# Kernel tuning notes

Measured on AMD Instinct MI355X. Metric: run time of the kernel, lower is better.

The kernel has to match this reference:

```python
import jax, jax.numpy as jnp
import numpy as np

N, E, IN, ED, HID, B, K = 50000, 800000, 128, 64, 256, 128, 1000


def setup_inputs() -> dict:
    key = jax.random.key(0)
    ks = jax.random.split(key, 16)

    def lin(k, fi, fo):
        k1, k2 = jax.random.split(k)
        s = 1.0 / np.sqrt(fi)
        return (jax.random.uniform(k1, (fi, fo), jnp.float32, -s, s),
                jax.random.uniform(k2, (fo,), jnp.float32, -s, s))

    We, be = lin(ks[0], ED, IN)        # GINEConv edge projection edge_dim -> in_channels
    W1, b1 = lin(ks[1], IN, HID)       # GINE nn layer 1
    W2, b2 = lin(ks[2], HID, HID)      # GINE nn layer 2
    Wg1, bg1 = lin(ks[3], HID, 128)    # gate_nn layer 1
    Wg2, bg2 = lin(ks[4], 128, 1)      # gate_nn layer 2
    Wh, bh = lin(ks[5], HID, K)        # head

    x = jax.random.normal(ks[6], (N, IN), jnp.float32)
    edge_index = jax.random.randint(ks[7], (2, E), 0, N, jnp.int64)
    edge_attr = jax.random.normal(ks[8], (E, ED), jnp.float32)
    batch = jnp.sort(jax.random.randint(ks[9], (N,), 0, B, jnp.int64))

    return {"x": x, "edge_index": edge_index, "edge_attr": edge_attr, "batch": batch,
            "We": We, "be": be, "W1": W1, "b1": b1, "W2": W2, "b2": b2,
            "Wg1": Wg1, "bg1": bg1, "Wg2": Wg2, "bg2": bg2, "Wh": Wh, "bh": bh}


def reference(x, edge_index, edge_attr, batch, We, be, W1, b1, W2, b2,
              Wg1, bg1, Wg2, bg2, Wh, bh):
    src, dst = edge_index[0], edge_index[1]
    # GINEConv message: ReLU(x_j + Lin(edge_attr)), scatter-add to dst (eps=0)
    e = edge_attr @ We + be                      # [E, IN]
    m = jax.nn.relu(x[src] + e)                  # [E, IN]
    agg = jax.ops.segment_sum(m, dst, num_segments=N)  # [N, IN]
    h = x + agg                                  # (1+eps)*x + agg, eps=0
    h = jax.nn.relu(h @ W1 + b1) @ W2 + b2       # [N, HID]
    # GlobalAttention: segment softmax of gate over graphs, weighted sum
    gate = jax.nn.relu(h @ Wg1 + bg1) @ Wg2 + bg2            # [N, 1]
    gmax = jax.ops.segment_max(gate, batch, num_segments=B)  # [B, 1]
    a = jnp.exp(gate - gmax[batch])
    denom = jax.ops.segment_sum(a, batch, num_segments=B)    # [B, 1]
    attn = a / denom[batch]
    pooled = jax.ops.segment_sum(attn * h, batch, num_segments=B)  # [B, HID]
    logits = pooled @ Wh + bh                    # [B, K]
    return (logits, pooled)
```

## Files before the change

### kernel.cpp

```cpp
#include <hip/hip_runtime.h>
#include <stdint.h>

#define NN    50000
#define EE    800000
#define IN_C  128
#define ED_C  64
#define HID_C 256
#define BB    128
#define KK    1000
#define G1_C  128
#define NV    50176


typedef __attribute__((ext_vector_type(8))) short bfrag;
typedef __attribute__((ext_vector_type(4))) float f4acc;

__device__ __forceinline__ unsigned short f2bs(float f){
  unsigned u = __float_as_uint(f);
  return (unsigned short)((u + 0x7fffu + ((u >> 16) & 1u)) >> 16);
}
__device__ __forceinline__ float bs2f(unsigned short s){
  return __uint_as_float(((unsigned)s) << 16);
}

__device__ __forceinline__ void atomicMaxFloat(float* addr, float val){
  int old = __float_as_int(*addr);
  while (__int_as_float(old) < val){
    int assumed = old;
    old = atomicCAS((int*)addr, assumed, __float_as_int(val));
    if (old == assumed) break;
  }
}

__global__ __launch_bounds__(256) void k_prep(
    const float* __restrict__ We, const float* __restrict__ W1,
    const float* __restrict__ W2, const float* __restrict__ Wg1,
    unsigned short* __restrict__ Wet, unsigned short* __restrict__ W1t,
    unsigned short* __restrict__ W2t, unsigned short* __restrict__ Wg1t)
{
  int i = blockIdx.x * 256 + threadIdx.x;
  if (i < 128 * 64){ int c = i >> 6, k = i & 63;  Wet[i]  = f2bs(We[k * 128 + c]); }
  if (i < 256 * 128){ int n = i >> 7, k = i & 127; W1t[i]  = f2bs(W1[k * 256 + n]); }
  if (i < 256 * 256){ int n = i >> 8, k = i & 255; W2t[i]  = f2bs(W2[k * 256 + n]); }
  if (i < 128 * 256){ int n = i >> 8, k = i & 255; Wg1t[i] = f2bs(Wg1[k * 128 + n]); }
}

__global__ __launch_bounds__(256) void k_init(float* __restrict__ agg,
                                              int* __restrict__ cnt,
                                              int* __restrict__ fill,
                                              int* __restrict__ aux,
                                              float* __restrict__ gmax,
                                              float* __restrict__ denom,
                                              float* __restrict__ pooled){
  size_t i = (size_t)blockIdx.x * 256 + threadIdx.x;
  if (i < (size_t)NN * IN_C) agg[i] = 0.f;
  if (i < NV){ cnt[i] = 0; fill[i] = 0; }
  if (i < 256) aux[i] = 0;
  if (i < BB){ gmax[i] = -1e30f; denom[i] = 0.f; }
  if (i < BB * HID_C) pooled[i] = 0.f;
}

__global__ __launch_bounds__(256) void k_hist(const int* __restrict__ ei,
                                              int* __restrict__ cnt){
  int e = blockIdx.x * 256 + threadIdx.x;
  if (e < EE) atomicAdd(&cnt[ei[EE + e]], 1);
}

__global__ __launch_bounds__(256) void k_scan1(const int* __restrict__ cnt,
                                               int* __restrict__ off,
                                               int* __restrict__ aux){
  __shared__ int s[256];
  int t = threadIdx.x, i = blockIdx.x * 256 + t;
  int val = cnt[i];
  s[t] = val; __syncthreads();
#pragma unroll
  for (int o = 1; o < 256; o <<= 1){
    int v = (t >= o) ? s[t - o] : 0;
    __syncthreads();
    s[t] += v;
    __syncthreads();
  }
  off[i] = s[t] - val;
  if (t == 255) aux[blockIdx.x] = s[255];
}

__global__ __launch_bounds__(256) void k_scan2(int* __restrict__ aux){
  __shared__ int s[256];
  int t = threadIdx.x;
  int val = aux[t];
  s[t] = val; __syncthreads();
#pragma unroll
  for (int o = 1; o < 256; o <<= 1){
    int v = (t >= o) ? s[t - o] : 0;
    __syncthreads();
    s[t] += v;
    __syncthreads();
  }
  aux[t] = s[t] - val;
}

__global__ __launch_bounds__(256) void k_scan3(int* __restrict__ off,
                                               const int* __restrict__ aux){
  int i = blockIdx.x * 256 + threadIdx.x;
  off[i] += aux[blockIdx.x];
}

__global__ __launch_bounds__(256) void k_scatter(const int* __restrict__ ei,
                                                 const int* __restrict__ off,
                                                 int* __restrict__ fill,
                                                 uint4* __restrict__ sorted){
  int e = blockIdx.x * 256 + threadIdx.x;
  if (e < EE){
    int s = ei[e], d = ei[EE + e];
    int pos = off[d] + atomicAdd(&fill[d], 1);
    sorted[pos] = make_uint4((unsigned)e, (unsigned)s, (unsigned)d, 0u);
  }
}

__global__ __launch_bounds__(256, 2) void k_edge2(
    const float* __restrict__ x, const uint4* __restrict__ sorted,
    const float* __restrict__ edge_attr,
    const unsigned short* __restrict__ Wet, const float* __restrict__ be,
    float* __restrict__ agg)
{
  __shared__ float msgS[128 * 132];
  __shared__ uint4 sE[128];
  __shared__ unsigned long long maskS[2];
  __shared__ int runStart[132];
  __shared__ int nRunsS;
  unsigned short* eaS = (unsigned short*)msgS;

  const int tid = threadIdx.x;
  const int e0 = blockIdx.x * 128;
  if (tid < 128) sE[tid] = sorted[e0 + tid];
  __syncthreads();

  const int xrow = tid >> 1;
  const int xc0 = (tid & 1) * 64;
  const float* xptr = x + (size_t)((int)sE[xrow].y) * IN_C + xc0;
  float4 xr[16];
#pragma unroll
  for (int j = 0; j < 16; ++j) xr[j] = *(const float4*)(xptr + j * 4);

  if (tid < 128){
    bool flag = (tid == 0) || ((int)sE[tid].z != (int)sE[tid - 1].z);
    unsigned long long m = __ballot(flag);
    if ((tid & 63) == 0) maskS[tid >> 6] = m;
  }

#pragma unroll
  for (int t = 0; t < 8; ++t){
    int f4 = t * 256 + tid;
    int er = f4 >> 4;
    int kk = (f4 & 15) * 4;
    int eid = (int)sE[er].x;
    const float4 v = *(const float4*)(edge_attr + (size_t)eid * ED_C + kk);
    unsigned p0 = (unsigned)f2bs(v.x) | ((unsigned)f2bs(v.y) << 16);
    unsigned p1 = (unsigned)f2bs(v.z) | ((unsigned)f2bs(v.w) << 16);
    *(uint2*)&eaS[er * 72 + kk] = make_uint2(p0, p1);
  }
  __syncthreads();

  if (tid < 128){
    int lane = tid & 63, wvi = tid >> 6;
    unsigned long long mw = maskS[wvi];
    int pre = __popcll(mw & ((1ull << lane) - 1ull)) + (wvi ? __popcll(maskS[0]) : 0);
    if ((mw >> lane) & 1ull) runStart[pre] = tid;
    if (tid == 0){
      int nr = __popcll(maskS[0]) + __popcll(maskS[1]);
      nRunsS = nr;
      runStart[nr] = 128;
    }
  }

  const int lane = tid & 63, wv = tid >> 6;
  const int q = lane >> 4, l15 = lane & 15;

  f4acc acc[2][8];
  const f4acc zz = {0.f, 0.f, 0.f, 0.f};
#pragma unroll
  for (int mt = 0; mt < 2; ++mt)
#pragma unroll
    for (int nt = 0; nt < 8; ++nt) acc[mt][nt] = zz;

#pragma unroll
  for (int ks = 0; ks < 2; ++ks){
    bfrag a[2], b[8];
#pragma unroll
    for (int mt = 0; mt < 2; ++mt){
      int m = wv * 32 + mt * 16 + l15;
      a[mt] = *(const bfrag*)&eaS[m * 72 + ks * 32 + q * 8];
    }
#pragma unroll
    for (int nt = 0; nt < 8; ++nt){
      int c = nt * 16 + l15;
      b[nt] = *(const bfrag*)(Wet + c * ED_C + ks * 32 + q * 8);
    }
#pragma unroll
    for (int mt = 0; mt < 2; ++mt)
#pragma unroll
      for (int nt = 0; nt < 8; ++nt)
        acc[mt][nt] = __builtin_amdgcn_mfma_f32_16x16x32_bf16(a[mt], b[nt], acc[mt][nt], 0, 0, 0);
  }

  float bev[8];
#pragma unroll
  for (int nt = 0; nt < 8; ++nt) bev[nt] = be[nt * 16 + l15];

  __syncthreads();

#pragma unroll
  for (int mt = 0; mt < 2; ++mt){
    const int g = wv * 32 + mt * 16 + q * 4;
#pragma unroll
    for (int nt = 0; nt < 8; ++nt){
      int c = nt * 16 + l15;
#pragma unroll
      for (int r = 0; r < 4; ++r)
        msgS[(g + r) * 132 + c] = acc[mt][nt][r] + bev[nt];
    }
  }
  __syncthreads();

  {
    float* mr = &msgS[xrow * 132 + xc0];
#pragma unroll
    for (int j = 0; j < 16; ++j){
      float4 w = *(float4*)(mr + j * 4);
      const float4 v = xr[j];
      w.x = fmaxf(w.x + v.x, 0.f);
      w.y = fmaxf(w.y + v.y, 0.f);
      w.z = fmaxf(w.z + v.z, 0.f);
      w.w = fmaxf(w.w + v.w, 0.f);
      *(float4*)(mr + j * 4) = w;
    }
  }
  __syncthreads();

  {
    const int col = tid & 127;
    const int h = tid >> 7;
    const int nR = nRunsS;
    for (int i = h; i < nR; i += 2){
      int s = runStart[i], e = runStart[i + 1];
      int dst = (int)sE[s].z;
      float run = 0.f;
      for (int r = s; r < e; ++r) run += msgS[r * 132 + col];
      size_t a = (size_t)dst * IN_C + col;
      if (s == 0 || e == 128) atomicAdd(&agg[a], run);
      else                    agg[a] = run;
    }
  }
}

__global__ __launch_bounds__(256) void k_h0(const float* __restrict__ agg,
                                            const float* __restrict__ x,
                                            unsigned short* __restrict__ h0b){
  int i = blockIdx.x * 256 + threadIdx.x;
  if (i < NN * IN_C) h0b[i] = f2bs(agg[i] + x[i]);
}

template<int K, bool RELU, bool OF32, bool OB16>
__global__ __launch_bounds__(256) void k_gemm(
    const unsigned short* __restrict__ A, const unsigned short* __restrict__ Wt,
    const float* __restrict__ bias, float* __restrict__ outf,
    unsigned short* __restrict__ outb, int M, int Ntot)
{
  __shared__ unsigned short aS[64 * 40];
  __shared__ unsigned short bS[128 * 40];
  const int tid = threadIdx.x;
  const int lane = tid & 63, wv = tid >> 6;
  const int wi = wv >> 1, wj = wv & 1;
  const int q = lane >> 4, l15 = lane & 15;
  const int mb0 = blockIdx.x * 64;
  const int nb0 = blockIdx.y * 128;
  const int arow = tid >> 2, achk = tid & 3;

  f4acc acc[2][4];
  const f4acc zz = {0.f, 0.f, 0.f, 0.f};
#pragma unroll
  for (int mt = 0; mt < 2; ++mt)
#pragma unroll
    for (int nt = 0; nt < 4; ++nt) acc[mt][nt] = zz;

  for (int ks = 0; ks < K / 32; ++ks){
    {
      int m = mb0 + arow; if (m >= M) m = M - 1;
      const uint4 v = *(const uint4*)(A + (size_t)m * K + ks * 32 + achk * 8);
      *(uint4*)&aS[arow * 40 + achk * 8] = v;
    }
#pragma unroll
    for (int i = 0; i < 2; ++i){
      int idx = i * 256 + tid;
      int row = idx >> 2, chk = idx & 3;
      const uint4 v = *(const uint4*)(Wt + (size_t)(nb0 + row) * K + ks * 32 + chk * 8);
      *(uint4*)&bS[row * 40 + chk * 8] = v;
    }
    __syncthreads();
    bfrag a[2], b[4];
#pragma unroll
    for (int mt = 0; mt < 2; ++mt)
      a[mt] = *(const bfrag*)&aS[(wi * 32 + mt * 16 + l15) * 40 + q * 8];
#pragma unroll
    for (int nt = 0; nt < 4; ++nt)
      b[nt] = *(const bfrag*)&bS[(wj * 64 + nt * 16 + l15) * 40 + q * 8];
#pragma unroll
    for (int mt = 0; mt < 2; ++mt)
#pragma unroll
      for (int nt = 0; nt < 4; ++nt)
        acc[mt][nt] = __builtin_amdgcn_mfma_f32_16x16x32_bf16(a[mt], b[nt], acc[mt][nt], 0, 0, 0);
    __syncthreads();
  }

  const int mb = mb0 + wi * 32;
  const int nb = nb0 + wj * 64;
#pragma unroll
  for (int nt = 0; nt < 4; ++nt){
    int c = nb + nt * 16 + l15;
    float bv = bias[c];
#pragma unroll
    for (int mt = 0; mt < 2; ++mt){
#pragma unroll
      for (int r = 0; r < 4; ++r){
        int m = mb + mt * 16 + q * 4 + r;
        if (m < M){
          float v = acc[mt][nt][r] + bv;
          if (RELU) v = v > 0.f ? v : 0.f;
          if (OF32) outf[(size_t)m * Ntot + c] = v;
          if (OB16) outb[(size_t)m * Ntot + c] = f2bs(v);
        }
      }
    }
  }
}

__global__ __launch_bounds__(256) void k_gate2(const float* __restrict__ g1,
                                               const float* __restrict__ Wg2,
                                               const float* __restrict__ bg2,
                                               float* __restrict__ gate, int nrows){
  const int lane = threadIdx.x & 63, wv = threadIdx.x >> 6;
  const float2 w2 = *(const float2*)(Wg2 + lane * 2);
  const float bg = bg2[0];
  for (int r = blockIdx.x * 4 + wv; r < nrows; r += gridDim.x * 4){
    const float2 a2 = *(const float2*)(g1 + (size_t)r * G1_C + lane * 2);
    float p = a2.x * w2.x + a2.y * w2.y;
#pragma unroll
    for (int off = 32; off > 0; off >>= 1) p += __shfl_down(p, off);
    if (lane == 0) gate[r] = p + bg;
  }
}

__global__ __launch_bounds__(256) void k_gmax(const float* __restrict__ gate,
                                              const int* __restrict__ batch,
                                              float* __restrict__ gmax, int nrows){
  __shared__ float red[256];
  const int tid = threadIdx.x;
  const int n0 = blockIdx.x * 256;
  const int n = n0 + tid;
  const int nlast = (n0 + 255 < nrows) ? n0 + 255 : nrows - 1;
  const int bmin = batch[n0], bmax = batch[nlast];
  float val = -3e38f; int b = bmax;
  if (n < nrows){ b = batch[n]; val = gate[n]; }
  for (int bb = bmin; bb <= bmax; ++bb){
    red[tid] = (b == bb) ? val : -3e38f;
    __syncthreads();
    for (int s = 128; s > 0; s >>= 1){
      if (tid < s) red[tid] = fmaxf(red[tid], red[tid + s]);
      __syncthreads();
    }
    if (tid == 0 && red[0] > -1e37f) atomicMaxFloat(&gmax[bb], red[0]);
    __syncthreads();
  }
}

__global__ __launch_bounds__(256) void k_expsum(const float* __restrict__ gate,
                                                const int* __restrict__ batch,
                                                const float* __restrict__ gmax,
                                                float* __restrict__ aexp,
                                                float* __restrict__ denom, int nrows){
  __shared__ float red[256];
  const int tid = threadIdx.x;
  const int n0 = blockIdx.x * 256;
  const int n = n0 + tid;
  const int nlast = (n0 + 255 < nrows) ? n0 + 255 : nrows - 1;
  const int bmin = batch[n0], bmax = batch[nlast];
  float val = 0.f; int b = bmax;
  if (n < nrows){
    b = batch[n];
    val = expf(gate[n] - gmax[b]);
    aexp[n] = val;
  }
  for (int bb = bmin; bb <= bmax; ++bb){
    red[tid] = (b == bb) ? val : 0.f;
    __syncthreads();
    for (int s = 128; s > 0; s >>= 1){
      if (tid < s) red[tid] += red[tid + s];
      __syncthreads();
    }
    if (tid == 0 && red[0] != 0.f) atomicAdd(&denom[bb], red[0]);
    __syncthreads();
  }
}

__global__ __launch_bounds__(256) void k_pool(const unsigned short* __restrict__ h2b,
                                              const float* __restrict__ aexp,
                                              const float* __restrict__ denom,
                                              const int* __restrict__ batch,
                                              float* __restrict__ pooled, int nrows){
  const int c = threadIdx.x;
  const int n0 = blockIdx.x * 256;
  int n1 = n0 + 256; if (n1 > nrows) n1 = nrows;
  float acc = 0.f;
  int curb = batch[n0];
  for (int n = n0; n < n1; ++n){
    int b = batch[n];
    if (b != curb){
      atomicAdd(&pooled[(size_t)curb * HID_C + c], acc);
      acc = 0.f; curb = b;
    }
    float wgt = aexp[n] / denom[b];
    acc = fmaf(wgt, bs2f(h2b[(size_t)n * HID_C + c]), acc);
  }
  atomicAdd(&pooled[(size_t)curb * HID_C + c], acc);
}

__global__ __launch_bounds__(256) void k_head(const float* __restrict__ pooled,
                                              const float* __restrict__ Wh,
                                              const float* __restrict__ bh,
                                              float* __restrict__ out_logits,
                                              float* __restrict__ out_pooled){
  __shared__ float p[HID_C];
  const int b = blockIdx.x, t = threadIdx.x;
  float pv = pooled[(size_t)b * HID_C + t];
  p[t] = pv;
  out_pooled[(size_t)b * HID_C + t] = pv;
  __syncthreads();
  for (int c = t; c < KK; c += 256){
    float acc = bh[c];
#pragma unroll 8
    for (int k = 0; k < HID_C; ++k)
      acc = fmaf(p[k], Wh[k * KK + c], acc);
    out_logits[(size_t)b * KK + c] = acc;
  }
}

extern "C" void kernel_launch(void* const* d_in, const int* in_sizes, int n_in,
                              void* d_out, int out_size, void* d_ws, size_t ws_size,
                              hipStream_t stream) {
  const float* x   = (const float*)d_in[0];
  const int*   ei  = (const int*)d_in[1];
  const float* ea  = (const float*)d_in[2];
  const int*   batch = (const int*)d_in[3];
  const float* We  = (const float*)d_in[4];
  const float* be  = (const float*)d_in[5];
  const float* W1  = (const float*)d_in[6];
  const float* b1  = (const float*)d_in[7];
  const float* W2  = (const float*)d_in[8];
  const float* b2  = (const float*)d_in[9];
  const float* Wg1 = (const float*)d_in[10];
  const float* bg1 = (const float*)d_in[11];
  const float* Wg2 = (const float*)d_in[12];
  const float* bg2 = (const float*)d_in[13];
  const float* Wh  = (const float*)d_in[14];
  const float* bh  = (const float*)d_in[15];

  float* out_logits = (float*)d_out;
  float* out_pooled = out_logits + (size_t)BB * KK;

  float* agg    = (float*)d_ws;
  float* gate   = agg   + (size_t)NN * IN_C;
  float* aexp   = gate  + NN;
  float* gmax   = aexp  + NN;
  float* denom  = gmax  + BB;
  float* pooled = denom + BB;
  float* fend   = pooled + (size_t)BB * HID_C;
  unsigned short* h0b  = (unsigned short*)fend;
  unsigned short* h1b  = h0b + (size_t)NN * IN_C;
  unsigned short* h2b  = h1b + (size_t)NN * HID_C;
  unsigned short* Wet  = h2b + (size_t)NN * HID_C;
  unsigned short* W1t  = Wet + 128 * 64;
  unsigned short* W2t  = W1t + 256 * 128;
  unsigned short* Wg1t = W2t + 256 * 256;
  float* g1f = agg;
  uint4* sorted = (uint4*)h1b;
  int* cnt  = (int*)(sorted + EE);
  int* off  = cnt + NV;
  int* fill = off + NV;
  int* aux  = fill + NV;

  k_prep<<<256, 256, 0, stream>>>(We, W1, W2, Wg1, Wet, W1t, W2t, Wg1t);
  k_init<<<(NN * IN_C + 255) / 256, 256, 0, stream>>>(agg, cnt, fill, aux, gmax, denom, pooled);
  k_hist   <<<(EE + 255) / 256, 256, 0, stream>>>(ei, cnt);
  k_scan1  <<<NV / 256, 256, 0, stream>>>(cnt, off, aux);
  k_scan2  <<<1, 256, 0, stream>>>(aux);
  k_scan3  <<<NV / 256, 256, 0, stream>>>(off, aux);
  k_scatter<<<(EE + 255) / 256, 256, 0, stream>>>(ei, off, fill, sorted);
  k_edge2<<<EE / 128, 256, 0, stream>>>(x, sorted, ea, Wet, be, agg);
  k_h0<<<(NN * IN_C + 255) / 256, 256, 0, stream>>>(agg, x, h0b);
  k_gemm<128, true,  false, true ><<<dim3(782, 2), 256, 0, stream>>>(h0b, W1t, b1, (float*)0, h1b, NN, HID_C);
  k_gemm<256, false, false, true ><<<dim3(782, 2), 256, 0, stream>>>(h1b, W2t, b2, (float*)0, h2b, NN, HID_C);
  k_gemm<256, true,  true,  false><<<dim3(782, 1), 256, 0, stream>>>(h2b, Wg1t, bg1, g1f, (unsigned short*)0, NN, G1_C);
  k_gate2<<<3125, 256, 0, stream>>>(g1f, Wg2, bg2, gate, NN);
  k_gmax  <<<(NN + 255) / 256, 256, 0, stream>>>(gate, batch, gmax, NN);
  k_expsum<<<(NN + 255) / 256, 256, 0, stream>>>(gate, batch, gmax, aexp, denom, NN);
  k_pool  <<<(NN + 255) / 256, 256, 0, stream>>>(h2b, aexp, denom, batch, pooled, NN);
  k_head<<<BB, 256, 0, stream>>>(pooled, Wh, bh, out_logits, out_pooled);
}
```

Baseline: 749.9 us.

## Halve edge tile to 64 edges per block and raise occupancy in edge kernel

The edge message kernel now handles 64 sorted edges per block instead of 128, with each wave owning one 16-row MFMA tile. Shared memory and register use drop, and launch bounds rise to 4 blocks per SIMD, so more blocks stay resident to hide gather latency. Run detection is folded into a single ballot, and the barrier between the accumulator store and the ReLU pass is removed because each wave now works only on its own rows. In exchange, twice as many blocks run, the Wet fragments are reloaded per block, and more runs cross tile boundaries, which means more atomic adds into agg.

```diff
diff --git a/kernel.cpp b/kernel.cpp
--- a/kernel.cpp
+++ b/kernel.cpp
@@ -117,39 +117,36 @@
   }
 }
 
-__global__ __launch_bounds__(256, 2) void k_edge2(
+__global__ __launch_bounds__(256, 4) void k_edge2(
     const float* __restrict__ x, const uint4* __restrict__ sorted,
     const float* __restrict__ edge_attr,
     const unsigned short* __restrict__ Wet, const float* __restrict__ be,
     float* __restrict__ agg)
 {
-  __shared__ float msgS[128 * 132];
-  __shared__ uint4 sE[128];
-  __shared__ unsigned long long maskS[2];
-  __shared__ int runStart[132];
+  __shared__ float msgS[64 * 132];
+  __shared__ uint4 sE[64];
+  __shared__ int runStart[66];
   __shared__ int nRunsS;
   unsigned short* eaS = (unsigned short*)msgS;
 
   const int tid = threadIdx.x;
-  const int e0 = blockIdx.x * 128;
-  if (tid < 128) sE[tid] = sorted[e0 + tid];
+  const int e0 = blockIdx.x * 64;
+  if (tid < 64) sE[tid] = sorted[e0 + tid];
   __syncthreads();
 
-  const int xrow = tid >> 1;
-  const int xc0 = (tid & 1) * 64;
+  const int lane = tid & 63, wv = tid >> 6;
+  const int q = lane >> 4, l15 = lane & 15;
+  const int g0 = wv * 16;
+
+  const int xrow = g0 + (lane >> 2);
+  const int xc0 = (lane & 3) * 32;
   const float* xptr = x + (size_t)((int)sE[xrow].y) * IN_C + xc0;
-  float4 xr[16];
-#pragma unroll
-  for (int j = 0; j < 16; ++j) xr[j] = *(const float4*)(xptr + j * 4);
-
-  if (tid < 128){
-    bool flag = (tid == 0) || ((int)sE[tid].z != (int)sE[tid - 1].z);
-    unsigned long long m = __ballot(flag);
-    if ((tid & 63) == 0) maskS[tid >> 6] = m;
-  }
-
-#pragma unroll
-  for (int t = 0; t < 8; ++t){
+  float4 xr[8];
+#pragma unroll
+  for (int j = 0; j < 8; ++j) xr[j] = *(const float4*)(xptr + j * 4);
+
+#pragma unroll
+  for (int t = 0; t < 4; ++t){
     int f4 = t * 256 + tid;
     int er = f4 >> 4;
     int kk = (f4 & 15) * 4;
@@ -159,48 +156,34 @@
     unsigned p1 = (unsigned)f2bs(v.z) | ((unsigned)f2bs(v.w) << 16);
     *(uint2*)&eaS[er * 72 + kk] = make_uint2(p0, p1);
   }
+
+  if (tid < 64){
+    bool flag = (tid == 0) || ((int)sE[tid].z != (int)sE[tid - 1].z);
+    unsigned long long m = __ballot(flag);
+    int pre = __popcll(m & ((1ull << tid) - 1ull));
+    if ((m >> tid) & 1ull) runStart[pre] = tid;
+    if (tid == 0){
+      int nr = __popcll(m);
+      nRunsS = nr;
+      runStart[nr] = 64;
+    }
+  }
   __syncthreads();
 
-  if (tid < 128){
-    int lane = tid & 63, wvi = tid >> 6;
-    unsigned long long mw = maskS[wvi];
-    int pre = __popcll(mw & ((1ull << lane) - 1ull)) + (wvi ? __popcll(maskS[0]) : 0);
-    if ((mw >> lane) & 1ull) runStart[pre] = tid;
-    if (tid == 0){
-      int nr = __popcll(maskS[0]) + __popcll(maskS[1]);
-      nRunsS = nr;
-      runStart[nr] = 128;
-    }
-  }
-
-  const int lane = tid & 63, wv = tid >> 6;
-  const int q = lane >> 4, l15 = lane & 15;
-
-  f4acc acc[2][8];
+  f4acc acc[8];
   const f4acc zz = {0.f, 0.f, 0.f, 0.f};
 #pragma unroll
-  for (int mt = 0; mt < 2; ++mt)
-#pragma unroll
-    for (int nt = 0; nt < 8; ++nt) acc[mt][nt] = zz;
+  for (int nt = 0; nt < 8; ++nt) acc[nt] = zz;
 
 #pragma unroll
   for (int ks = 0; ks < 2; ++ks){
-    bfrag a[2], b[8];
-#pragma unroll
-    for (int mt = 0; mt < 2; ++mt){
-      int m = wv * 32 + mt * 16 + l15;
-      a[mt] = *(const bfrag*)&eaS[m * 72 + ks * 32 + q * 8];
-    }
+    bfrag a = *(const bfrag*)&eaS[(g0 + l15) * 72 + ks * 32 + q * 8];
 #pragma unroll
     for (int nt = 0; nt < 8; ++nt){
       int c = nt * 16 + l15;
-      b[nt] = *(const bfrag*)(Wet + c * ED_C + ks * 32 + q * 8);
-    }
-#pragma unroll
-    for (int mt = 0; mt < 2; ++mt)
-#pragma unroll
-      for (int nt = 0; nt < 8; ++nt)
-        acc[mt][nt] = __builtin_amdgcn_mfma_f32_16x16x32_bf16(a[mt], b[nt], acc[mt][nt], 0, 0, 0);
+      bfrag b = *(const bfrag*)(Wet + c * ED_C + ks * 32 + q * 8);
+      acc[nt] = __builtin_amdgcn_mfma_f32_16x16x32_bf16(a, b, acc[nt], 0, 0, 0);
+    }
   }
 
   float bev[8];
@@ -210,22 +193,17 @@
   __syncthreads();
 
 #pragma unroll
-  for (int mt = 0; mt < 2; ++mt){
-    const int g = wv * 32 + mt * 16 + q * 4;
-#pragma unroll
-    for (int nt = 0; nt < 8; ++nt){
-      int c = nt * 16 + l15;
-#pragma unroll
-      for (int r = 0; r < 4; ++r)
-        msgS[(g + r) * 132 + c] = acc[mt][nt][r] + bev[nt];
-    }
-  }
-  __syncthreads();
+  for (int nt = 0; nt < 8; ++nt){
+    int c = nt * 16 + l15;
+#pragma unroll
+    for (int r = 0; r < 4; ++r)
+      msgS[(g0 + q * 4 + r) * 132 + c] = acc[nt][r] + bev[nt];
+  }
 
   {
     float* mr = &msgS[xrow * 132 + xc0];
 #pragma unroll
-    for (int j = 0; j < 16; ++j){
+    for (int j = 0; j < 8; ++j){
       float4 w = *(float4*)(mr + j * 4);
       const float4 v = xr[j];
       w.x = fmaxf(w.x + v.x, 0.f);
@@ -247,8 +225,8 @@
       float run = 0.f;
       for (int r = s; r < e; ++r) run += msgS[r * 132 + col];
       size_t a = (size_t)dst * IN_C + col;
-      if (s == 0 || e == 128) atomicAdd(&agg[a], run);
-      else                    agg[a] = run;
+      if (s == 0 || e == 64) atomicAdd(&agg[a], run);
+      else                   agg[a] = run;
     }
   }
 }
@@ -495,7 +473,7 @@
   k_scan2  <<<1, 256, 0, stream>>>(aux);
   k_scan3  <<<NV / 256, 256, 0, stream>>>(off, aux);
   k_scatter<<<(EE + 255) / 256, 256, 0, stream>>>(ei, off, fill, sorted);
-  k_edge2<<<EE / 128, 256, 0, stream>>>(x, sorted, ea, Wet, be, agg);
+  k_edge2<<<EE / 64, 256, 0, stream>>>(x, sorted, ea, Wet, be, agg);
   k_h0<<<(NN * IN_C + 255) / 256, 256, 0, stream>>>(agg, x, h0b);
   k_gemm<128, true,  false, true ><<<dim3(782, 2), 256, 0, stream>>>(h0b, W1t, b1, (float*)0, h1b, NN, HID_C);
   k_gemm<256, false, false, true ><<<dim3(782, 2), 256, 0, stream>>>(h1b, W2t, b2, (float*)0, h2b, NN, HID_C);
```

After: 751.0 us. Within noise of the previous version (+0.1%).
